# Performance work log

Measured on AMD Instinct MI355X. Metric: run time of the kernel, lower is better.

## Reference

```python
import math
import jax, jax.numpy as jnp
import numpy as np

EMBED = 1024
HIDDEN = 1024
HEADS = 16


def setup_inputs() -> dict:
    key = jax.random.key(0)
    ks = jax.random.split(key, 9)
    B, S = 1, 4096
    s = 1.0 / math.sqrt(EMBED)
    return {
        "x": jax.random.normal(ks[0], (B, S, EMBED), dtype=jnp.float32),
        "Wq": jax.random.normal(ks[1], (EMBED, HIDDEN), dtype=jnp.float32) * s,
        "bq": jnp.zeros((HIDDEN,), dtype=jnp.float32),
        "Wk": jax.random.normal(ks[2], (EMBED, HIDDEN), dtype=jnp.float32) * s,
        "bk": jnp.zeros((HIDDEN,), dtype=jnp.float32),
        "Wv": jax.random.normal(ks[3], (EMBED, HIDDEN), dtype=jnp.float32) * s,
        "bv": jnp.zeros((HIDDEN,), dtype=jnp.float32),
        "Wo": jax.random.normal(ks[4], (EMBED, HIDDEN), dtype=jnp.float32) * s,
        "bo": jnp.zeros((HIDDEN,), dtype=jnp.float32),
    }


def reference(x, Wq, bq, Wk, bk, Wv, bv, Wo, bo):
    B, S, _ = x.shape
    Hd = HIDDEN // HEADS
    # projections: [B,S,hidden] -> [B,H,S,hd]
    def split_heads(t):
        return t.reshape(B, S, HEADS, Hd).transpose(0, 2, 1, 3)
    q = split_heads(x @ Wq + bq)
    k = split_heads(x @ Wk + bk)
    v = split_heads(x @ Wv + bv)
    scale = 1.0 / math.sqrt(EMBED / HEADS)
    scores = jnp.einsum("bhqd,bhkd->bhqk", q, k) * scale  # [B,H,S,S]
    attn = jax.nn.softmax(scores, axis=-1)
    ctx = jnp.einsum("bhqk,bhkd->bhqd", attn, v)
    ctx = ctx.transpose(0, 2, 1, 3).reshape(B, S, HIDDEN)
    return ctx @ Wo + bo
```

## Files before the change

### kernel.cpp

```cpp
#include <hip/hip_runtime.h>
#include <hip/hip_bf16.h>
#include <math.h>

typedef __bf16 bf16;
typedef bf16  bf16x2 __attribute__((ext_vector_type(2)));
typedef bf16  bf16x4 __attribute__((ext_vector_type(4)));
typedef bf16  bf16x8 __attribute__((ext_vector_type(8)));
typedef float f32x4  __attribute__((ext_vector_type(4)));
typedef float f32x16 __attribute__((ext_vector_type(16)));
typedef unsigned uint4v __attribute__((ext_vector_type(4)));

#define MFMA16(a, b, c) __builtin_amdgcn_mfma_f32_16x16x32_bf16((a), (b), (c), 0, 0, 0)
#define MFMA32(a, b, c) __builtin_amdgcn_mfma_f32_32x32x16_bf16((a), (b), (c), 0, 0, 0)

static constexpr int S  = 4096;
static constexpr int E  = 1024;
static constexpr int NH = 16;
static constexpr int HD = 64;

__device__ __forceinline__ void gload16(const bf16* g, bf16* l) {
    __builtin_amdgcn_global_load_lds(
        (const __attribute__((address_space(1))) void*)g,
        (__attribute__((address_space(3))) void*)l, 16, 0, 0);
}

__global__ void convert_f32_bf16(const float* __restrict__ in, bf16* __restrict__ out, int n) {
    int i = (blockIdx.x * blockDim.x + threadIdx.x) * 8;
    if (i < n) {
        float4 v0 = *(const float4*)(in + i);
        float4 v1 = *(const float4*)(in + i + 4);
        bf16x8 o = { (bf16)v0.x, (bf16)v0.y, (bf16)v0.z, (bf16)v0.w,
                     (bf16)v1.x, (bf16)v1.y, (bf16)v1.z, (bf16)v1.w };
        *(bf16x8*)(out + i) = o;
    }
}

__global__ void transpose_w(const float* __restrict__ W0, const float* __restrict__ W1,
                            const float* __restrict__ W2, const float* __restrict__ W3,
                            bf16* __restrict__ T0, bf16* __restrict__ T1,
                            bf16* __restrict__ T2, bf16* __restrict__ T3) {
    const float* W; bf16* T;
    switch (blockIdx.z) {
        case 0: W = W0; T = T0; break;
        case 1: W = W1; T = T1; break;
        case 2: W = W2; T = T2; break;
        default: W = W3; T = T3; break;
    }
    __shared__ float tile[64][65];
    int k0 = blockIdx.x * 64, n0 = blockIdx.y * 64;
    #pragma unroll
    for (int i = 0; i < 16; i++) {
        int idx = threadIdx.x + i * 256;
        int r = idx >> 6, c = idx & 63;
        tile[r][c] = W[(k0 + r) * E + n0 + c];
    }
    __syncthreads();
    #pragma unroll
    for (int i = 0; i < 8; i++) {
        int idx = threadIdx.x + i * 256;
        int r = idx >> 5, c2 = (idx & 31) * 2;
        bf16x2 v = { (bf16)tile[c2][r], (bf16)tile[c2 + 1][r] };
        *(bf16x2*)(T + (n0 + r) * E + k0 + c2) = v;
    }
}

template<int MODE>
__global__ __launch_bounds__(256) void gemm128(const bf16* __restrict__ A,
                                               const bf16* __restrict__ BT,
                                               const float* __restrict__ b0,
                                               const float* __restrict__ b1,
                                               const float* __restrict__ b2,
                                               void* __restrict__ out0,
                                               void* __restrict__ out1,
                                               void* __restrict__ out2,
                                               float qscale) {
    __shared__ __align__(16) bf16 Als[2][128 * 32];
    __shared__ __align__(16) bf16 Bls[2][128 * 32];
    const int tid = threadIdx.x, lane = tid & 63, w = tid >> 6;
    const int wm = w >> 1, wn = w & 1;
    const int m0 = blockIdx.x * 128, n0 = blockIdx.y * 128;
    const int ln = lane & 15, g = lane >> 4;

    const bf16* Ag = A  + (size_t)(m0 + w * 32 + (lane >> 2)) * E + (lane & 3) * 8;
    const bf16* Bg = BT + (size_t)(n0 + w * 32 + (lane >> 2)) * E + (lane & 3) * 8;

    auto stage = [&](int buf, int kt) {
        #pragma unroll
        for (int j = 0; j < 2; j++) {
            gload16(Ag + j * 16 * E + kt, (bf16*)((char*)&Als[buf][0] + w * 2048 + j * 1024));
            gload16(Bg + j * 16 * E + kt, (bf16*)((char*)&Bls[buf][0] + w * 2048 + j * 1024));
        }
    };

    f32x4 acc[4][4] = {};
    stage(0, 0);
    __syncthreads();
    int cur = 0;
    for (int kt = 0; kt < E; kt += 32, cur ^= 1) {
        if (kt + 32 < E) stage(cur ^ 1, kt + 32);
        bf16x8 af[4], bfr[4];
        #pragma unroll
        for (int i = 0; i < 4; i++) {
            af[i]  = *(const bf16x8*)(&Als[cur][0] + (wm * 64 + i * 16 + ln) * 32 + g * 8);
            bfr[i] = *(const bf16x8*)(&Bls[cur][0] + (wn * 64 + i * 16 + ln) * 32 + g * 8);
        }
        __builtin_amdgcn_s_setprio(1);
        #pragma unroll
        for (int mi = 0; mi < 4; mi++)
            #pragma unroll
            for (int bj = 0; bj < 4; bj++)
                acc[mi][bj] = MFMA16(af[mi], bfr[bj], acc[mi][bj]);
        __builtin_amdgcn_s_setprio(0);
        __syncthreads();
    }

    if (MODE == 0) {
        const int proj = n0 >> 10;
        const float* bias = proj == 0 ? b0 : (proj == 1 ? b1 : b2);
        bf16* outp = (bf16*)(proj == 0 ? out0 : (proj == 1 ? out1 : out2));
        const float osc = proj == 0 ? qscale : 1.0f;
        if (proj < 2) {
            #pragma unroll
            for (int bj = 0; bj < 4; bj++) {
                const int n = n0 + wn * 64 + bj * 16 + ln;
                const int nn = n & 1023, hh = nn >> 6, dd = nn & 63;
                const float bb = bias[nn];
                #pragma unroll
                for (int mi = 0; mi < 4; mi++) {
                    const int m = m0 + wm * 64 + mi * 16 + g * 4;
                    #pragma unroll
                    for (int r = 0; r < 4; r++)
                        outp[((size_t)hh * S + m + r) * HD + dd] = (bf16)((acc[mi][bj][r] + bb) * osc);
                }
            }
        } else {
            #pragma unroll
            for (int bj = 0; bj < 4; bj++) {
                const int n = n0 + wn * 64 + bj * 16 + ln;
                const int nn = n & 1023;
                const float bb = bias[nn];
                #pragma unroll
                for (int mi = 0; mi < 4; mi++) {
                    const int m = m0 + wm * 64 + mi * 16 + g * 4;
                    bf16x4 vv = { (bf16)(acc[mi][bj][0] + bb), (bf16)(acc[mi][bj][1] + bb),
                                  (bf16)(acc[mi][bj][2] + bb), (bf16)(acc[mi][bj][3] + bb) };
                    *(bf16x4*)(outp + (size_t)nn * S + m) = vv;
                }
            }
        }
    } else {
        float* outp = (float*)out0;
        #pragma unroll
        for (int bj = 0; bj < 4; bj++) {
            const int n = n0 + wn * 64 + bj * 16 + ln;
            const float bb = b0[n];
            #pragma unroll
            for (int mi = 0; mi < 4; mi++) {
                const int m = m0 + wm * 64 + mi * 16 + g * 4;
                #pragma unroll
                for (int r = 0; r < 4; r++)
                    outp[(size_t)(m + r) * E + n] = acc[mi][bj][r] + bb;
            }
        }
    }
}

__global__ __launch_bounds__(512) void flash_attn5(const bf16* __restrict__ Qh,
                                                   const bf16* __restrict__ Kh,
                                                   const bf16* __restrict__ Vt,
                                                   bf16* __restrict__ ctx) {
    __shared__ __align__(16) char smem[65536];
    const int tid = threadIdx.x, lane = tid & 63, w = tid >> 6;
    const int w4 = w & 3, kvh = w >> 2;
    const int h = blockIdx.y, qb = blockIdx.x;
    const int l31 = lane & 31, h5 = lane >> 5;
    const int q_global = qb * 128 + w4 * 32 + l31;

    const bf16* Qbase = Qh + ((size_t)h * S + q_global) * HD;
    bf16x8 qf[4];
    #pragma unroll
    for (int t = 0; t < 4; t++) qf[t] = *(const bf16x8*)(Qbase + t * 16 + h5 * 8);

    const int srow = w4 * 16 + (lane >> 3);
    const int scol = ((lane & 7) ^ (lane >> 3)) * 8;
    const int swz  = (lane & 7) << 4;

    char* const Kb0 = smem + kvh * 16384;
    char* const Vb0 = smem + 32768 + kvh * 16384;

    auto stage = [&](int buf, int kv) {
        #pragma unroll
        for (int j = 0; j < 2; j++) {
            gload16(Kh + ((size_t)h * S + kv + srow + j * 8) * HD + scol,
                    (bf16*)(Kb0 + buf * 8192 + w4 * 2048 + j * 1024));
            gload16(Vt + ((size_t)(h * HD + srow + j * 8)) * S + kv + scol,
                    (bf16*)(Vb0 + buf * 8192 + w4 * 2048 + j * 1024));
        }
    };

    auto exppack = [&](const f32x16& s, bf16x8& pa, bf16x8& pc, float& rs) {
        unsigned d[8];
        #pragma unroll
        for (int i = 0; i < 8; i++) {
            float e0 = __builtin_amdgcn_exp2f(s[2 * i]);
            float e1 = __builtin_amdgcn_exp2f(s[2 * i + 1]);
            rs += e0 + e1;
            asm("v_cvt_pk_bf16_f32 %0, %1, %2" : "=v"(d[i]) : "v"(e0), "v"(e1));
        }
        asm volatile("v_permlane32_swap_b32 %0, %1" : "+v"(d[0]), "+v"(d[2]));
        asm volatile("v_permlane32_swap_b32 %0, %1" : "+v"(d[1]), "+v"(d[3]));
        asm volatile("v_permlane32_swap_b32 %0, %1" : "+v"(d[4]), "+v"(d[6]));
        asm volatile("v_permlane32_swap_b32 %0, %1" : "+v"(d[5]), "+v"(d[7]));
        uint4v fa = { d[0], d[1], d[2], d[3] }, fb = { d[4], d[5], d[6], d[7] };
        pa = __builtin_bit_cast(bf16x8, fa);
        pc = __builtin_bit_cast(bf16x8, fb);
    };

    f32x16 o0 = {}, o1 = {};
    float l_i = 0.f;
    const int kv0 = kvh * (S / 2);
    constexpr int NT = S / 128;

    stage(0, kv0);
    for (int t = 0; t < NT; t++) {
        const int cur = t & 1;
        __syncthreads();
        if (t + 1 < NT) stage(cur ^ 1, kv0 + (t + 1) * 64);

        const char* Kb = Kb0 + cur * 8192;
        const char* Vb = Vb0 + cur * 8192;

        f32x16 s0 = {}, s1 = {};
        __builtin_amdgcn_s_setprio(1);
        #pragma unroll
        for (int t4 = 0; t4 < 4; t4++) {
            const int cb = (t4 * 32 + h5 * 16) ^ swz;
            bf16x8 k0 = *(const bf16x8*)(Kb + l31 * 128 + cb);
            bf16x8 k1 = *(const bf16x8*)(Kb + (32 + l31) * 128 + cb);
            s0 = MFMA32(k0, qf[t4], s0);
            s1 = MFMA32(k1, qf[t4], s1);
        }
        __builtin_amdgcn_s_setprio(0);

        bf16x8 pb[4];
        float rs = 0.f;
        exppack(s0, pb[0], pb[1], rs);
        exppack(s1, pb[2], pb[3], rs);
        l_i += rs;

        __builtin_amdgcn_s_setprio(1);
        #pragma unroll
        for (int ks = 0; ks < 4; ks++) {
            const int cb = (ks * 32 + h5 * 16) ^ swz;
            bf16x8 va  = *(const bf16x8*)(Vb + l31 * 128 + cb);
            bf16x8 vb2 = *(const bf16x8*)(Vb + (32 + l31) * 128 + cb);
            o0 = MFMA32(va, pb[ks], o0);
            o1 = MFMA32(vb2, pb[ks], o1);
        }
        __builtin_amdgcn_s_setprio(0);
    }

    __syncthreads();
    float* const lr  = (float*)(smem + 32768);
    float* const orr = (float*)smem + w4 * 2048;
    if (w >= 4) {
        lr[w4 * 64 + lane] = l_i;
        #pragma unroll
        for (int r = 0; r < 16; r++) orr[r * 64 + lane]        = o0[r];
        #pragma unroll
        for (int r = 0; r < 16; r++) orr[(16 + r) * 64 + lane] = o1[r];
    }
    __syncthreads();
    if (w < 4) {
        l_i += lr[w4 * 64 + lane];
        #pragma unroll
        for (int r = 0; r < 16; r++) o0[r] += orr[r * 64 + lane];
        #pragma unroll
        for (int r = 0; r < 16; r++) o1[r] += orr[(16 + r) * 64 + lane];
        l_i += __shfl_xor(l_i, 32);
        const float inv = 1.f / l_i;
        bf16* cbase = ctx + (size_t)q_global * E + h * HD;
        #pragma unroll
        for (int dg = 0; dg < 2; dg++) {
            const f32x16& o = dg ? o1 : o0;
            #pragma unroll
            for (int rq = 0; rq < 4; rq++) {
                bf16x4 ov = { (bf16)(o[rq * 4 + 0] * inv), (bf16)(o[rq * 4 + 1] * inv),
                              (bf16)(o[rq * 4 + 2] * inv), (bf16)(o[rq * 4 + 3] * inv) };
                *(bf16x4*)(cbase + dg * 32 + rq * 8 + h5 * 4) = ov;
            }
        }
    }
}

extern "C" void kernel_launch(void* const* d_in, const int* in_sizes, int n_in,
                              void* d_out, int out_size, void* d_ws, size_t ws_size,
                              hipStream_t stream) {
    const float* x  = (const float*)d_in[0];
    const float* Wq = (const float*)d_in[1];
    const float* bq = (const float*)d_in[2];
    const float* Wk = (const float*)d_in[3];
    const float* bk = (const float*)d_in[4];
    const float* Wv = (const float*)d_in[5];
    const float* bv = (const float*)d_in[6];
    const float* Wo = (const float*)d_in[7];
    const float* bo = (const float*)d_in[8];

    char* ws = (char*)d_ws;
    const size_t MB = 1u << 20;
    bf16* xb   = (bf16*)(ws + 0 * MB);
    bf16* Wcat = (bf16*)(ws + 8 * MB);
    bf16* tq   = Wcat;
    bf16* tk   = Wcat + 1024 * 1024;
    bf16* tv   = Wcat + 2048 * 1024;
    bf16* to   = (bf16*)(ws + 14 * MB);
    bf16* Qh   = (bf16*)(ws + 16 * MB);
    bf16* Kh   = (bf16*)(ws + 24 * MB);
    bf16* Vt   = (bf16*)(ws + 32 * MB);
    bf16* ctx  = (bf16*)(ws + 40 * MB);

    const float qscale = 0.125f * 1.44269504088896f;

    convert_f32_bf16<<<dim3(S * E / 2048), 256, 0, stream>>>(x, xb, S * E);
    transpose_w<<<dim3(16, 16, 4), 256, 0, stream>>>(Wq, Wk, Wv, Wo, tq, tk, tv, to);

    gemm128<0><<<dim3(S / 128, 3072 / 128), 256, 0, stream>>>(
        xb, Wcat, bq, bk, bv, Qh, Kh, Vt, qscale);

    flash_attn5<<<dim3(S / 128, NH), 512, 0, stream>>>(Qh, Kh, Vt, ctx);

    gemm128<1><<<dim3(S / 128, E / 128), 256, 0, stream>>>(
        ctx, to, bo, nullptr, nullptr, d_out, nullptr, nullptr, 1.0f);
}
```

Baseline: 152.0 us.

## Use 256x256 swizzled LDS tiles for QKV GEMM and explicit waitcnt pipelining

Replaces the 128x128 QKV projection GEMM with a 512-thread kernel computing 256x256 tiles over 64-wide K steps. It uses 128KB of dynamic LDS with an XOR swizzle to avoid bank conflicts, and more MFMAs per LDS load for better operand reuse. Both GEMMs swap __syncthreads for explicit vmcnt/lgkmcnt waits plus raw barriers, so the next stage's loads stay in flight during compute. The trade-off is a grid of only 192 blocks and one block per CU at high register use, which may underfill the GPU. The 128KB dynamic LDS request may also need an attribute to allow it.

```diff
diff --git a/kernel.cpp b/kernel.cpp
--- a/kernel.cpp
+++ b/kernel.cpp
@@ -64,16 +64,121 @@
     }
 }
 
-template<int MODE>
-__global__ __launch_bounds__(256) void gemm128(const bf16* __restrict__ A,
-                                               const bf16* __restrict__ BT,
-                                               const float* __restrict__ b0,
-                                               const float* __restrict__ b1,
-                                               const float* __restrict__ b2,
-                                               void* __restrict__ out0,
-                                               void* __restrict__ out1,
-                                               void* __restrict__ out2,
-                                               float qscale) {
+__global__ __launch_bounds__(512) void gemm256_qkv(const bf16* __restrict__ A,
+                                                   const bf16* __restrict__ BT,
+                                                   const float* __restrict__ b0,
+                                                   const float* __restrict__ b1,
+                                                   const float* __restrict__ b2,
+                                                   bf16* __restrict__ outQ,
+                                                   bf16* __restrict__ outK,
+                                                   bf16* __restrict__ outV,
+                                                   float qscale) {
+    extern __shared__ char lds[];
+    const int tid = threadIdx.x, lane = tid & 63, w = tid >> 6;
+    const int wm = w >> 2, wn = w & 3;
+    const int m0 = blockIdx.x * 256, n0 = blockIdx.y * 256;
+    const int ln = lane & 15, g = lane >> 4;
+    const int swz = (ln & 7) << 4;
+
+    const int sr   = w * 16 + (lane >> 3);
+    const int scol = ((lane & 7) ^ ((lane >> 3) & 7)) * 8;
+    const bf16* Ag = A  + (size_t)(m0 + sr) * E + scol;
+    const bf16* Bg = BT + (size_t)(n0 + sr) * E + scol;
+
+    auto stageT = [&](int buf, int t) {
+        const int kc = t * 64;
+        #pragma unroll
+        for (int h = 0; h < 2; h++)
+            #pragma unroll
+            for (int j = 0; j < 2; j++)
+                gload16(Ag + (size_t)(h * 128 + j * 8) * E + kc,
+                        (bf16*)(lds + (buf * 2 + h) * 16384 + (w * 16 + j * 8) * 128));
+        #pragma unroll
+        for (int h = 0; h < 2; h++)
+            #pragma unroll
+            for (int j = 0; j < 2; j++)
+                gload16(Bg + (size_t)(h * 128 + j * 8) * E + kc,
+                        (bf16*)(lds + 65536 + (buf * 2 + h) * 16384 + (w * 16 + j * 8) * 128));
+    };
+
+    f32x4 acc[8][4] = {};
+    const int brow = (wn & 1) * 64;
+    constexpr int NT = E / 64;
+
+    stageT(0, 0);
+    for (int i = 0; i < NT; i++) {
+        const int cur = i & 1;
+        if (i + 1 < NT) {
+            stageT(cur ^ 1, i + 1);
+            asm volatile("s_waitcnt vmcnt(8)" ::: "memory");
+        } else {
+            asm volatile("s_waitcnt vmcnt(0)" ::: "memory");
+        }
+        __builtin_amdgcn_s_barrier();
+        __builtin_amdgcn_sched_barrier(0);
+
+        const char* Ab = lds + (cur * 2 + wm) * 16384;
+        const char* Bb = lds + 65536 + (cur * 2 + (wn >> 1)) * 16384;
+        #pragma unroll
+        for (int kh = 0; kh < 2; kh++) {
+            const int cb = kh * 64 + g * 16;
+            bf16x8 bfr[4];
+            #pragma unroll
+            for (int bj = 0; bj < 4; bj++)
+                bfr[bj] = *(const bf16x8*)(Bb + (brow + bj * 16 + ln) * 128 + (cb ^ swz));
+            __builtin_amdgcn_s_setprio(1);
+            #pragma unroll
+            for (int mi = 0; mi < 8; mi++) {
+                bf16x8 af = *(const bf16x8*)(Ab + (mi * 16 + ln) * 128 + (cb ^ swz));
+                #pragma unroll
+                for (int bj = 0; bj < 4; bj++)
+                    acc[mi][bj] = MFMA16(af, bfr[bj], acc[mi][bj]);
+            }
+            __builtin_amdgcn_s_setprio(0);
+        }
+        asm volatile("s_waitcnt lgkmcnt(0)" ::: "memory");
+        __builtin_amdgcn_sched_barrier(0);
+        __builtin_amdgcn_s_barrier();
+    }
+
+    const int proj = n0 >> 10;
+    const float* bias = proj == 0 ? b0 : (proj == 1 ? b1 : b2);
+    bf16* outp = proj == 0 ? outQ : (proj == 1 ? outK : outV);
+    const float osc = proj == 0 ? qscale : 1.0f;
+    if (proj < 2) {
+        #pragma unroll
+        for (int bj = 0; bj < 4; bj++) {
+            const int nn = (n0 + wn * 64 + bj * 16 + ln) & 1023;
+            const int hh = nn >> 6, dd = nn & 63;
+            const float bb = bias[nn];
+            #pragma unroll
+            for (int mi = 0; mi < 8; mi++) {
+                const int m = m0 + wm * 128 + mi * 16 + g * 4;
+                #pragma unroll
+                for (int r = 0; r < 4; r++)
+                    outp[((size_t)hh * S + m + r) * HD + dd] = (bf16)((acc[mi][bj][r] + bb) * osc);
+            }
+        }
+    } else {
+        #pragma unroll
+        for (int bj = 0; bj < 4; bj++) {
+            const int nn = (n0 + wn * 64 + bj * 16 + ln) & 1023;
+            const float bb = bias[nn];
+            #pragma unroll
+            for (int mi = 0; mi < 8; mi++) {
+                const int m = m0 + wm * 128 + mi * 16 + g * 4;
+                bf16x4 vv = { (bf16)(acc[mi][bj][0] + bb), (bf16)(acc[mi][bj][1] + bb),
+                              (bf16)(acc[mi][bj][2] + bb), (bf16)(acc[mi][bj][3] + bb) };
+                *(bf16x4*)(outp + (size_t)nn * S + m) = vv;
+            }
+        }
+    }
+}
+
+__global__ __launch_bounds__(256) void gemm_o(const bf16* __restrict__ A,
+                                              const bf16* __restrict__ BT,
+                                              const float* __restrict__ bias,
+                                              float* __restrict__ outp) {
     __shared__ __align__(16) bf16 Als[2][128 * 32];
     __shared__ __align__(16) bf16 Bls[2][128 * 32];
     const int tid = threadIdx.x, lane = tid & 63, w = tid >> 6;
@@ -94,10 +199,17 @@
 
     f32x4 acc[4][4] = {};
     stage(0, 0);
-    __syncthreads();
     int cur = 0;
     for (int kt = 0; kt < E; kt += 32, cur ^= 1) {
-        if (kt + 32 < E) stage(cur ^ 1, kt + 32);
+        if (kt + 32 < E) {
+            stage(cur ^ 1, kt + 32);
+            asm volatile("s_waitcnt vmcnt(4)" ::: "memory");
+        } else {
+            asm volatile("s_waitcnt vmcnt(0)" ::: "memory");
+        }
+        __builtin_amdgcn_s_barrier();
+        __builtin_amdgcn_sched_barrier(0);
+
         bf16x8 af[4], bfr[4];
         #pragma unroll
         for (int i = 0; i < 4; i++) {
@@ -111,56 +223,21 @@
             for (int bj = 0; bj < 4; bj++)
                 acc[mi][bj] = MFMA16(af[mi], bfr[bj], acc[mi][bj]);
         __builtin_amdgcn_s_setprio(0);
-        __syncthreads();
-    }
-
-    if (MODE == 0) {
-        const int proj = n0 >> 10;
-        const float* bias = proj == 0 ? b0 : (proj == 1 ? b1 : b2);
-        bf16* outp = (bf16*)(proj == 0 ? out0 : (proj == 1 ? out1 : out2));
-        const float osc = proj == 0 ? qscale : 1.0f;
-        if (proj < 2) {
-            #pragma unroll
-            for (int bj = 0; bj < 4; bj++) {
-                const int n = n0 + wn * 64 + bj * 16 + ln;
-                const int nn = n & 1023, hh = nn >> 6, dd = nn & 63;
-                const float bb = bias[nn];
-                #pragma unroll
-                for (int mi = 0; mi < 4; mi++) {
-                    const int m = m0 + wm * 64 + mi * 16 + g * 4;
-                    #pragma unroll
-                    for (int r = 0; r < 4; r++)
-                        outp[((size_t)hh * S + m + r) * HD + dd] = (bf16)((acc[mi][bj][r] + bb) * osc);
-                }
-            }
-        } else {
-            #pragma unroll
-            for (int bj = 0; bj < 4; bj++) {
-                const int n = n0 + wn * 64 + bj * 16 + ln;
-                const int nn = n & 1023;
-                const float bb = bias[nn];
-                #pragma unroll
-                for (int mi = 0; mi < 4; mi++) {
-                    const int m = m0 + wm * 64 + mi * 16 + g * 4;
-                    bf16x4 vv = { (bf16)(acc[mi][bj][0] + bb), (bf16)(acc[mi][bj][1] + bb),
-                                  (bf16)(acc[mi][bj][2] + bb), (bf16)(acc[mi][bj][3] + bb) };
-                    *(bf16x4*)(outp + (size_t)nn * S + m) = vv;
-                }
-            }
-        }
-    } else {
-        float* outp = (float*)out0;
-        #pragma unroll
-        for (int bj = 0; bj < 4; bj++) {
-            const int n = n0 + wn * 64 + bj * 16 + ln;
-            const float bb = b0[n];
-            #pragma unroll
-            for (int mi = 0; mi < 4; mi++) {
-                const int m = m0 + wm * 64 + mi * 16 + g * 4;
-                #pragma unroll
-                for (int r = 0; r < 4; r++)
-                    outp[(size_t)(m + r) * E + n] = acc[mi][bj][r] + bb;
-            }
+        asm volatile("s_waitcnt lgkmcnt(0)" ::: "memory");
+        __builtin_amdgcn_sched_barrier(0);
+        __builtin_amdgcn_s_barrier();
+    }
+
+    #pragma unroll
+    for (int bj = 0; bj < 4; bj++) {
+        const int n = n0 + wn * 64 + bj * 16 + ln;
+        const float bb = bias[n];
+        #pragma unroll
+        for (int mi = 0; mi < 4; mi++) {
+            const int m = m0 + wm * 64 + mi * 16 + g * 4;
+            #pragma unroll
+            for (int r = 0; r < 4; r++)
+                outp[(size_t)(m + r) * E + n] = acc[mi][bj][r] + bb;
         }
     }
 }
@@ -324,11 +401,10 @@
     convert_f32_bf16<<<dim3(S * E / 2048), 256, 0, stream>>>(x, xb, S * E);
     transpose_w<<<dim3(16, 16, 4), 256, 0, stream>>>(Wq, Wk, Wv, Wo, tq, tk, tv, to);
 
-    gemm128<0><<<dim3(S / 128, 3072 / 128), 256, 0, stream>>>(
+    gemm256_qkv<<<dim3(S / 256, 3072 / 256), 512, 131072, stream>>>(
         xb, Wcat, bq, bk, bv, Qh, Kh, Vt, qscale);
 
     flash_attn5<<<dim3(S / 128, NH), 512, 0, stream>>>(Qh, Kh, Vt, ctx);
 
-    gemm128<1><<<dim3(S / 128, E / 128), 256, 0, stream>>>(
-        ctx, to, bo, nullptr, nullptr, d_out, nullptr, nullptr, 1.0f);
-}
+    gemm_o<<<dim3(S / 128, E / 128), 256, 0, stream>>>(ctx, to, bo, (float*)d_out);
+}
```

After: 146.8 us. 1.04x faster.

## Deepen GEMM K-tile to 64 with XOR-swizzled LDS and explicit vmcnt pipelining

Applied to the files above, without the earlier changes.

The projection and output GEMMs now stage K tiles of 64 instead of 32, which halves the number of barrier-separated iterations. The LDS layout is XOR-swizzled on the 16-byte column chunk to avoid bank conflicts on the 128-byte rows. Synchronisation now uses explicit s_waitcnt vmcnt(8) with raw s_barrier and sched_barrier, so the next tile's loads stay in flight while the current tile is computed. LDS use doubles to 64 KB per block, which may reduce occupancy.

```diff
diff --git a/kernel.cpp b/kernel.cpp
--- a/kernel.cpp
+++ b/kernel.cpp
@@ -65,53 +65,74 @@
 }
 
 template<int MODE>
-__global__ __launch_bounds__(256) void gemm128(const bf16* __restrict__ A,
-                                               const bf16* __restrict__ BT,
-                                               const float* __restrict__ b0,
-                                               const float* __restrict__ b1,
-                                               const float* __restrict__ b2,
-                                               void* __restrict__ out0,
-                                               void* __restrict__ out1,
-                                               void* __restrict__ out2,
-                                               float qscale) {
-    __shared__ __align__(16) bf16 Als[2][128 * 32];
-    __shared__ __align__(16) bf16 Bls[2][128 * 32];
+__global__ __launch_bounds__(256) void gemm128d(const bf16* __restrict__ A,
+                                                const bf16* __restrict__ BT,
+                                                const float* __restrict__ b0,
+                                                const float* __restrict__ b1,
+                                                const float* __restrict__ b2,
+                                                void* __restrict__ out0,
+                                                void* __restrict__ out1,
+                                                void* __restrict__ out2,
+                                                float qscale) {
+    __shared__ __align__(16) bf16 Als[2][128 * 64];
+    __shared__ __align__(16) bf16 Bls[2][128 * 64];
     const int tid = threadIdx.x, lane = tid & 63, w = tid >> 6;
     const int wm = w >> 1, wn = w & 1;
     const int m0 = blockIdx.x * 128, n0 = blockIdx.y * 128;
     const int ln = lane & 15, g = lane >> 4;
-
-    const bf16* Ag = A  + (size_t)(m0 + w * 32 + (lane >> 2)) * E + (lane & 3) * 8;
-    const bf16* Bg = BT + (size_t)(n0 + w * 32 + (lane >> 2)) * E + (lane & 3) * 8;
+    const int swz = (ln & 7) << 4;
+
+    const int scol = ((lane & 7) ^ ((lane >> 3) & 7)) * 8;
+    const bf16* Ag = A  + (size_t)(m0 + w * 32 + (lane >> 3)) * E + scol;
+    const bf16* Bg = BT + (size_t)(n0 + w * 32 + (lane >> 3)) * E + scol;
 
     auto stage = [&](int buf, int kt) {
         #pragma unroll
-        for (int j = 0; j < 2; j++) {
-            gload16(Ag + j * 16 * E + kt, (bf16*)((char*)&Als[buf][0] + w * 2048 + j * 1024));
-            gload16(Bg + j * 16 * E + kt, (bf16*)((char*)&Bls[buf][0] + w * 2048 + j * 1024));
-        }
+        for (int j = 0; j < 4; j++)
+            gload16(Ag + (size_t)j * 8 * E + kt,
+                    (bf16*)((char*)&Als[buf][0] + w * 4096 + j * 1024));
+        #pragma unroll
+        for (int j = 0; j < 4; j++)
+            gload16(Bg + (size_t)j * 8 * E + kt,
+                    (bf16*)((char*)&Bls[buf][0] + w * 4096 + j * 1024));
     };
 
     f32x4 acc[4][4] = {};
+    constexpr int NT = E / 64;
     stage(0, 0);
-    __syncthreads();
-    int cur = 0;
-    for (int kt = 0; kt < E; kt += 32, cur ^= 1) {
-        if (kt + 32 < E) stage(cur ^ 1, kt + 32);
-        bf16x8 af[4], bfr[4];
-        #pragma unroll
-        for (int i = 0; i < 4; i++) {
-            af[i]  = *(const bf16x8*)(&Als[cur][0] + (wm * 64 + i * 16 + ln) * 32 + g * 8);
-            bfr[i] = *(const bf16x8*)(&Bls[cur][0] + (wn * 64 + i * 16 + ln) * 32 + g * 8);
-        }
-        __builtin_amdgcn_s_setprio(1);
-        #pragma unroll
-        for (int mi = 0; mi < 4; mi++)
+    for (int t = 0; t < NT; t++) {
+        const int cur = t & 1;
+        if (t + 1 < NT) {
+            stage(cur ^ 1, (t + 1) * 64);
+            asm volatile("s_waitcnt vmcnt(8)" ::: "memory");
+        } else {
+            asm volatile("s_waitcnt vmcnt(0)" ::: "memory");
+        }
+        __builtin_amdgcn_s_barrier();
+        __builtin_amdgcn_sched_barrier(0);
+
+        const char* Ab = (const char*)&Als[cur][0];
+        const char* Bb = (const char*)&Bls[cur][0];
+        #pragma unroll
+        for (int kh = 0; kh < 2; kh++) {
+            const int cb = kh * 64 + g * 16;
+            bf16x8 bfr[4];
             #pragma unroll
             for (int bj = 0; bj < 4; bj++)
-                acc[mi][bj] = MFMA16(af[mi], bfr[bj], acc[mi][bj]);
-        __builtin_amdgcn_s_setprio(0);
-        __syncthreads();
+                bfr[bj] = *(const bf16x8*)(Bb + (wn * 64 + bj * 16 + ln) * 128 + (cb ^ swz));
+            __builtin_amdgcn_s_setprio(1);
+            #pragma unroll
+            for (int mi = 0; mi < 4; mi++) {
+                bf16x8 af = *(const bf16x8*)(Ab + (wm * 64 + mi * 16 + ln) * 128 + (cb ^ swz));
+                #pragma unroll
+                for (int bj = 0; bj < 4; bj++)
+                    acc[mi][bj] = MFMA16(af, bfr[bj], acc[mi][bj]);
+            }
+            __builtin_amdgcn_s_setprio(0);
+        }
+        asm volatile("s_waitcnt lgkmcnt(0)" ::: "memory");
+        __builtin_amdgcn_sched_barrier(0);
+        __builtin_amdgcn_s_barrier();
     }
 
     if (MODE == 0) {
@@ -122,8 +143,8 @@
         if (proj < 2) {
             #pragma unroll
             for (int bj = 0; bj < 4; bj++) {
-                const int n = n0 + wn * 64 + bj * 16 + ln;
-                const int nn = n & 1023, hh = nn >> 6, dd = nn & 63;
+                const int nn = (n0 + wn * 64 + bj * 16 + ln) & 1023;
+                const int hh = nn >> 6, dd = nn & 63;
                 const float bb = bias[nn];
                 #pragma unroll
                 for (int mi = 0; mi < 4; mi++) {
@@ -136,8 +157,7 @@
         } else {
             #pragma unroll
             for (int bj = 0; bj < 4; bj++) {
-                const int n = n0 + wn * 64 + bj * 16 + ln;
-                const int nn = n & 1023;
+                const int nn = (n0 + wn * 64 + bj * 16 + ln) & 1023;
                 const float bb = bias[nn];
                 #pragma unroll
                 for (int mi = 0; mi < 4; mi++) {
@@ -324,11 +344,11 @@
     convert_f32_bf16<<<dim3(S * E / 2048), 256, 0, stream>>>(x, xb, S * E);
     transpose_w<<<dim3(16, 16, 4), 256, 0, stream>>>(Wq, Wk, Wv, Wo, tq, tk, tv, to);
 
-    gemm128<0><<<dim3(S / 128, 3072 / 128), 256, 0, stream>>>(
+    gemm128d<0><<<dim3(S / 128, 3072 / 128), 256, 0, stream>>>(
         xb, Wcat, bq, bk, bv, Qh, Kh, Vt, qscale);
 
     flash_attn5<<<dim3(S / 128, NH), 512, 0, stream>>>(Qh, Kh, Vt, ctx);
 
-    gemm128<1><<<dim3(S / 128, E / 128), 256, 0, stream>>>(
+    gemm128d<1><<<dim3(S / 128, E / 128), 256, 0, stream>>>(
         ctx, to, bo, nullptr, nullptr, d_out, nullptr, nullptr, 1.0f);
 }
```

Result: no change. 150.9 us (-0.7%).
